# Kernel tuning notes

Measured on AMD Instinct MI355X. Metric: run time of the kernel, lower is better.

## Reference

```python
import jax, jax.numpy as jnp
import numpy as np

N, E, G = 50000, 800000, 500          # nodes, edges, graphs
NFEAT, NHID, EFEAT = 128, 128, 16
L, NCLASS = 4, 10
BN_EPS = 1e-5


def setup_inputs() -> dict:
    key = jax.random.key(0)
    ks = jax.random.split(key, 10)
    w = lambda k, shape: (jax.random.normal(k, shape, jnp.float32) * 0.05)
    return {
        "h": jax.random.normal(ks[0], (N, NFEAT), jnp.float32),
        "edge_attr": jax.random.normal(ks[1], (E, EFEAT), jnp.float32),
        "edge_index": jax.random.randint(ks[2], (2, E), 0, N),
        "edge_feat_mat": jnp.zeros((1,), jnp.int32),   # placeholder (unused by simplified conv)
        "pair_info": jnp.zeros((1,), jnp.int32),       # placeholder (unused by simplified conv)
        "batch": jnp.sort(jax.random.randint(ks[3], (N,), 0, G)),
        "emb_W": w(ks[4], (NFEAT, NHID)), "emb_b": jnp.zeros((NHID,), jnp.float32),
        "conv_W": w(ks[5], (L, NHID, NHID)), "conv_b": jnp.zeros((L, NHID), jnp.float32),
        "conv_We": w(ks[6], (L, EFEAT, NHID)), "conv_be": jnp.zeros((L, NHID), jnp.float32),
        "bn_gamma": jnp.ones((L, NHID), jnp.float32), "bn_beta": jnp.zeros((L, NHID), jnp.float32),
        "jk_W": w(ks[7], (L + 1, NHID, NCLASS)), "jk_b": jnp.zeros((L + 1, NCLASS), jnp.float32),
    }


def _conv(h, edge_attr, src, dst, W, b, We, be):
    # GIN-style message passing: gather src features, add projected edge feats,
    # scatter-add into dst, then a dense transform of (self + aggregate).
    msg = h[src] + edge_attr @ We + be                      # [E, NHID]
    agg = jax.ops.segment_sum(msg, dst, num_segments=h.shape[0])  # [N, NHID]
    return (h + agg) @ W + b


def _batch_norm(x, gamma, beta):
    mu = jnp.mean(x, axis=0)
    var = jnp.mean(jnp.square(x - mu), axis=0)  # biased, as in torch BN training
    return (x - mu) * jax.lax.rsqrt(var + BN_EPS) * gamma + beta


def reference(h, edge_attr, edge_index, edge_feat_mat, pair_info, batch,
              emb_W, emb_b, conv_W, conv_b, conv_We, conv_be,
              bn_gamma, bn_beta, jk_W, jk_b):
    src, dst = edge_index[0], edge_index[1]
    h = h @ emb_W + emb_b                                   # embedding_h
    h_list = [h]
    for layer in range(L):
        z = _conv(h, edge_attr, src, dst,
                  conv_W[layer], conv_b[layer], conv_We[layer], conv_be[layer])
        z = _batch_norm(z, bn_gamma[layer], bn_beta[layer])
        z = jax.nn.relu(z)
        h = z + h_list[layer]                               # residual (dropout p=0)
        h_list.append(h)
    # JK: sum of per-layer linear heads applied to global_add_pool
    out = jnp.zeros((G, NCLASS), jnp.float32)
    for layer in range(L + 1):
        pooled = jax.ops.segment_sum(h_list[layer], batch, num_segments=G)  # [G, NHID]
        out = out + pooled @ jk_W[layer] + jk_b[layer]
    return out
```

## Files before the change

kernel.cpp:

```cpp
#include <hip/hip_runtime.h>

#define NH 128
#define LAYERS 4
#define BW 128
#define CHUNK 4096

typedef __attribute__((ext_vector_type(8))) short short8;
typedef __attribute__((ext_vector_type(4))) float f32x4;

__device__ __forceinline__ unsigned short f2bf(float f) {
    unsigned u = __float_as_uint(f);
    u += 0x7fffu + ((u >> 16) & 1u);
    return (unsigned short)(u >> 16);
}
__device__ __forceinline__ float bflo(unsigned u) { return __uint_as_float(u << 16); }
__device__ __forceinline__ float bfhi(unsigned u) { return __uint_as_float(u & 0xffff0000u); }
__device__ __forceinline__ unsigned packbf(float x, float y) {
    return (unsigned)f2bf(x) | ((unsigned)f2bf(y) << 16);
}

__global__ __launch_bounds__(256) void bhist_kernel(const int* __restrict__ dst, int E,
                                                    int* __restrict__ gH, int NBKT, int NCH,
                                                    const int* __restrict__ batch,
                                                    int* __restrict__ gstart, int N, int G) {
    __shared__ int hist[512];
    int b = blockIdx.x, t = threadIdx.x;
    for (int i = t; i < NBKT; i += 256) hist[i] = 0;
    __syncthreads();
    int base = b * CHUNK, end = min(base + CHUNK, E);
    for (int e = base + t; e < end; e += 256)
        atomicAdd(&hist[dst[e] >> 7], 1);
    __syncthreads();
    for (int i = t; i < NBKT; i += 256) gH[i * NCH + b] = hist[i];

    for (int i = b * 256 + t; i < N; i += gridDim.x * 256) {
        int bb = batch[i];
        int prev = (i == 0) ? -1 : batch[i - 1];
        for (int g = prev + 1; g <= bb; ++g) gstart[g] = i;
        if (i == N - 1)
            for (int g = bb + 1; g <= G; ++g) gstart[g] = N;
    }
}

__global__ __launch_bounds__(256) void block_sum_kernel(const int* __restrict__ deg,
                                                        int* __restrict__ bsum, int n) {
    __shared__ int red[256];
    int t = threadIdx.x;
    int base = blockIdx.x * 1024;
    int s = 0;
#pragma unroll
    for (int i = 0; i < 4; ++i) {
        int idx = base + i * 256 + t;
        if (idx < n) s += deg[idx];
    }
    red[t] = s;
    __syncthreads();
    for (int off = 128; off > 0; off >>= 1) {
        if (t < off) red[t] += red[t + off];
        __syncthreads();
    }
    if (t == 0) bsum[blockIdx.x] = red[0];
}

__global__ __launch_bounds__(1024) void scan_partials_kernel(int* __restrict__ bsum, int nb,
                                                             int* __restrict__ total_out, int n) {
    __shared__ int part[1024];
    int t = threadIdx.x;
    int v = (t < nb) ? bsum[t] : 0;
    part[t] = v;
    __syncthreads();
    for (int off = 1; off < 1024; off <<= 1) {
        int u = (t >= off) ? part[t - off] : 0;
        __syncthreads();
        part[t] += u;
        __syncthreads();
    }
    if (t < nb) bsum[t] = part[t] - v;
    if (t == 1023) total_out[n] = part[1023];
}

__global__ __launch_bounds__(256) void local_scan_kernel(const int* __restrict__ deg,
                                                         const int* __restrict__ bsum,
                                                         int* __restrict__ outA, int n) {
    __shared__ int part[256];
    int t = threadIdx.x;
    int base = blockIdx.x * 1024 + t * 4;
    int v0 = 0, v1 = 0, v2 = 0, v3 = 0;
    if (base + 3 < n) {
        int4 v = *(const int4*)(deg + base);
        v0 = v.x; v1 = v.y; v2 = v.z; v3 = v.w;
    } else {
        if (base + 0 < n) v0 = deg[base + 0];
        if (base + 1 < n) v1 = deg[base + 1];
        if (base + 2 < n) v2 = deg[base + 2];
        if (base + 3 < n) v3 = deg[base + 3];
    }
    int tsum = v0 + v1 + v2 + v3;
    part[t] = tsum;
    __syncthreads();
    for (int off = 1; off < 256; off <<= 1) {
        int u = (t >= off) ? part[t - off] : 0;
        __syncthreads();
        part[t] += u;
        __syncthreads();
    }
    int run = bsum[blockIdx.x] + part[t] - tsum;
    int r0 = run, r1 = run + v0, r2 = r1 + v1, r3 = r2 + v2;
    if (base + 3 < n) {
        *(int4*)(outA + base) = make_int4(r0, r1, r2, r3);
    } else {
        if (base + 0 < n) outA[base + 0] = r0;
        if (base + 1 < n) outA[base + 1] = r1;
        if (base + 2 < n) outA[base + 2] = r2;
        if (base + 3 < n) outA[base + 3] = r3;
    }
}

__global__ __launch_bounds__(256) void bplace_kernel(const int* __restrict__ src,
                                                     const int* __restrict__ dst, int E,
                                                     const int* __restrict__ gOff,
                                                     int NBKT, int NCH,
                                                     int2* __restrict__ bkt) {
    __shared__ int cur[512];
    int b = blockIdx.x, t = threadIdx.x;
    for (int i = t; i < NBKT; i += 256) cur[i] = gOff[i * NCH + b];
    __syncthreads();
    int base = b * CHUNK, end = min(base + CHUNK, E);
    for (int e = base + t; e < end; e += 256) {
        int d = dst[e];
        int p = atomicAdd(&cur[d >> 7], 1);
        bkt[p] = make_int2(src[e], ((d & (BW - 1)) << 25) | e);
    }
}

__global__ __launch_bounds__(256) void bfinal_kernel(const int2* __restrict__ bkt,
                                                     const int* __restrict__ gOff, int NCH,
                                                     int* __restrict__ row_start,
                                                     int2* __restrict__ pk,
                                                     int N, int E) {
    __shared__ int cnt[BW], par[BW];
    int b = blockIdx.x, t = threadIdx.x;
    int s = gOff[b * NCH];
    int e = (b + 1 < (int)gridDim.x) ? gOff[(b + 1) * NCH] : E;
    if (t < BW) cnt[t] = 0;
    __syncthreads();
    for (int p = s + t; p < e; p += 256)
        atomicAdd(&cnt[(unsigned)bkt[p].y >> 25], 1);
    __syncthreads();
    if (t < BW) par[t] = cnt[t];
    __syncthreads();
    for (int off = 1; off < BW; off <<= 1) {
        int u = (t < BW && t >= off) ? par[t - off] : 0;
        __syncthreads();
        if (t < BW) par[t] += u;
        __syncthreads();
    }
    int node = b * BW + t;
    if (t < BW) {
        int excl = par[t] - cnt[t];
        if (node <= N) row_start[node] = s + excl;
        cnt[t] = s + excl;
    }
    if (b == 0 && t == 0) row_start[N] = E;
    __syncthreads();
    for (int p = s + t; p < e; p += 256) {
        int2 v = bkt[p];
        int dloc = (unsigned)v.y >> 25;
        int pos = atomicAdd(&cnt[dloc], 1);
        pk[pos] = make_int2(v.x, v.y & 0x1FFFFFF);
    }
}

__global__ __launch_bounds__(256) void easum_kernel(const float* __restrict__ edge_attr,
                                                    const int2* __restrict__ pk,
                                                    const int* __restrict__ row_start,
                                                    float* __restrict__ easum, int N) {
    int t = threadIdx.x;
    int node = blockIdx.x * 16 + (t >> 4);
    int k = t & 15;
    if (node >= N) return;
    int rs = row_start[node], re = row_start[node + 1];
    float acc = 0.f;
    for (int p = rs; p < re; ++p)
        acc += edge_attr[(size_t)pk[p].y * 16 + k];
    easum[node * 16 + k] = acc;
}

__global__ __launch_bounds__(256) void aggregate_kernel(
    const unsigned* __restrict__ hbfu, const int2* __restrict__ pk,
    const int* __restrict__ row_start, const float* __restrict__ easum,
    const float* __restrict__ We, const float* __restrict__ be,
    unsigned* __restrict__ xbfu, int N) {
    __shared__ float2 WeL[16 * 64];
    int t = threadIdx.x;
    const float2* Wg2 = (const float2*)We;
    for (int i = t; i < 16 * 64; i += 256) WeL[i] = Wg2[i];
    __syncthreads();

    int wave = t >> 6, lane = t & 63;
    int n = blockIdx.x * 4 + wave;
    if (n >= N) return;
    unsigned uself = hbfu[(size_t)n * 64 + lane];
    float2 acc = make_float2(bflo(uself), bfhi(uself));
    float2 acc2 = make_float2(0.f, 0.f);
    float2 acc3 = make_float2(0.f, 0.f);
    float2 acc4 = make_float2(0.f, 0.f);
    int rs = row_start[n], re = row_start[n + 1];
    float myea = (lane < 16) ? easum[n * 16 + lane] : 0.f;

    for (int base = rs; base < re; base += 64) {
        int cnt = min(64, re - base);
        int myS = (base + lane < re) ? pk[base + lane].x : 0;
        int j = 0;
        for (; j + 15 < cnt; j += 16) {
            int s0 = __shfl(myS, j);      int s1 = __shfl(myS, j + 1);
            int s2 = __shfl(myS, j + 2);  int s3 = __shfl(myS, j + 3);
            int s4 = __shfl(myS, j + 4);  int s5 = __shfl(myS, j + 5);
            int s6 = __shfl(myS, j + 6);  int s7 = __shfl(myS, j + 7);
            int s8 = __shfl(myS, j + 8);  int s9 = __shfl(myS, j + 9);
            int sa = __shfl(myS, j + 10); int sb = __shfl(myS, j + 11);
            int sc = __shfl(myS, j + 12); int sd = __shfl(myS, j + 13);
            int se = __shfl(myS, j + 14); int sf = __shfl(myS, j + 15);
            unsigned u0 = hbfu[(size_t)s0 * 64 + lane];
            unsigned u1 = hbfu[(size_t)s1 * 64 + lane];
            unsigned u2 = hbfu[(size_t)s2 * 64 + lane];
            unsigned u3 = hbfu[(size_t)s3 * 64 + lane];
            unsigned u4 = hbfu[(size_t)s4 * 64 + lane];
            unsigned u5 = hbfu[(size_t)s5 * 64 + lane];
            unsigned u6 = hbfu[(size_t)s6 * 64 + lane];
            unsigned u7 = hbfu[(size_t)s7 * 64 + lane];
            unsigned u8 = hbfu[(size_t)s8 * 64 + lane];
            unsigned u9 = hbfu[(size_t)s9 * 64 + lane];
            unsigned ua = hbfu[(size_t)sa * 64 + lane];
            unsigned ub = hbfu[(size_t)sb * 64 + lane];
            unsigned uc = hbfu[(size_t)sc * 64 + lane];
            unsigned ud = hbfu[(size_t)sd * 64 + lane];
            unsigned ue = hbfu[(size_t)se * 64 + lane];
            unsigned uf = hbfu[(size_t)sf * 64 + lane];
            acc.x  += bflo(u0) + bflo(u1) + bflo(u2) + bflo(u3);
            acc.y  += bfhi(u0) + bfhi(u1) + bfhi(u2) + bfhi(u3);
            acc2.x += bflo(u4) + bflo(u5) + bflo(u6) + bflo(u7);
            acc2.y += bfhi(u4) + bfhi(u5) + bfhi(u6) + bfhi(u7);
            acc3.x += bflo(u8) + bflo(u9) + bflo(ua) + bflo(ub);
            acc3.y += bfhi(u8) + bfhi(u9) + bfhi(ua) + bfhi(ub);
            acc4.x += bflo(uc) + bflo(ud) + bflo(ue) + bflo(uf);
            acc4.y += bfhi(uc) + bfhi(ud) + bfhi(ue) + bfhi(uf);
        }
        for (; j + 3 < cnt; j += 4) {
            int s0 = __shfl(myS, j);
            int s1 = __shfl(myS, j + 1);
            int s2 = __shfl(myS, j + 2);
            int s3 = __shfl(myS, j + 3);
            unsigned u0 = hbfu[(size_t)s0 * 64 + lane];
            unsigned u1 = hbfu[(size_t)s1 * 64 + lane];
            unsigned u2 = hbfu[(size_t)s2 * 64 + lane];
            unsigned u3 = hbfu[(size_t)s3 * 64 + lane];
            acc.x += bflo(u0) + bflo(u1) + bflo(u2) + bflo(u3);
            acc.y += bfhi(u0) + bfhi(u1) + bfhi(u2) + bfhi(u3);
        }
        for (; j < cnt; ++j) {
            int s = __shfl(myS, j);
            unsigned u = hbfu[(size_t)s * 64 + lane];
            acc.x += bflo(u);
            acc.y += bfhi(u);
        }
    }
    acc.x += (acc2.x + acc3.x) + acc4.x;
    acc.y += (acc2.y + acc3.y) + acc4.y;

    float degf = (float)(re - rs);
    float2 be2 = ((const float2*)be)[lane];
#pragma unroll
    for (int k = 0; k < 16; ++k) {
        float e = __shfl(myea, k);
        float2 w = WeL[k * 64 + lane];
        acc.x = fmaf(e, w.x, acc.x);
        acc.y = fmaf(e, w.y, acc.y);
    }
    acc.x += degf * be2.x;
    acc.y += degf * be2.y;
    xbfu[(size_t)n * 64 + lane] = packbf(acc.x, acc.y);
}

__global__ __launch_bounds__(256) void gemm_mfma_kernel(
    const unsigned short* __restrict__ Abf, const float* __restrict__ Af32,
    const float* __restrict__ W, const float* __restrict__ bias,
    float* __restrict__ Zf, unsigned short* __restrict__ Zbf,
    int N, float* __restrict__ bnsum, float* __restrict__ bnsumsq) {
    __shared__ unsigned short Wl[128 * 128];
    __shared__ float bnL[2 * NH];
    int t = threadIdx.x;
    for (int i = t; i < 128 * 64; i += 256) {
        float2 w2 = ((const float2*)W)[i];
        int k = i >> 6, n = (i & 63) * 2;
        int kc = k >> 5, quad = (k >> 3) & 3, j = k & 7;
        int base = (((n >> 4) * 4 + kc) * 4 + quad) * 128 + j;
        Wl[base + ((n & 15) << 3)] = f2bf(w2.x);
        Wl[base + (((n + 1) & 15) << 3)] = f2bf(w2.y);
    }
    if (t < 2 * NH) bnL[t] = 0.f;
    __syncthreads();

    int wave = t >> 6, lane = t & 63;
    int quad = lane >> 4, ln = lane & 15;
    int row0 = blockIdx.x * 128 + wave * 32;

    f32x4 acc[2][8];
#pragma unroll
    for (int nt = 0; nt < 8; ++nt) {
        float bv = bias[nt * 16 + ln];
        acc[0][nt] = (f32x4){bv, bv, bv, bv};
        acc[1][nt] = (f32x4){bv, bv, bv, bv};
    }

    for (int kc = 0; kc < 4; ++kc) {
        short8 afr[2];
        if (Af32) {
#pragma unroll
            for (int mt = 0; mt < 2; ++mt) {
                int ar = row0 + mt * 16 + ln; if (ar >= N) ar = N - 1;
                const float4* ap = (const float4*)(Af32 + (size_t)ar * NH + kc * 32 + quad * 8);
                float4 a0 = ap[0], a1 = ap[1];
                short8 v;
                v[0] = (short)f2bf(a0.x); v[1] = (short)f2bf(a0.y);
                v[2] = (short)f2bf(a0.z); v[3] = (short)f2bf(a0.w);
                v[4] = (short)f2bf(a1.x); v[5] = (short)f2bf(a1.y);
                v[6] = (short)f2bf(a1.z); v[7] = (short)f2bf(a1.w);
                afr[mt] = v;
            }
        } else {
#pragma unroll
            for (int mt = 0; mt < 2; ++mt) {
                int ar = row0 + mt * 16 + ln; if (ar >= N) ar = N - 1;
                afr[mt] = *(const short8*)(Abf + (size_t)ar * NH + kc * 32 + quad * 8);
            }
        }
#pragma unroll
        for (int nt = 0; nt < 8; ++nt) {
            short8 bfr = *(const short8*)(Wl + ((nt * 4 + kc) * 4 + quad) * 128 + ln * 8);
            acc[0][nt] = __builtin_amdgcn_mfma_f32_16x16x32_bf16(afr[0], bfr, acc[0][nt], 0, 0, 0);
            acc[1][nt] = __builtin_amdgcn_mfma_f32_16x16x32_bf16(afr[1], bfr, acc[1][nt], 0, 0, 0);
        }
    }

#pragma unroll
    for (int mt = 0; mt < 2; ++mt)
#pragma unroll
        for (int r = 0; r < 4; ++r) {
            int row = row0 + mt * 16 + quad * 4 + r;
            if (row < N) {
#pragma unroll
                for (int nt = 0; nt < 8; ++nt) {
                    int col = nt * 16 + ln;
                    float v = acc[mt][nt][r];
                    if (Zf) Zf[(size_t)row * NH + col] = v;
                    if (Zbf) Zbf[(size_t)row * NH + col] = f2bf(v);
                }
            }
        }

    if (bnsum) {
#pragma unroll
        for (int nt = 0; nt < 8; ++nt) {
            float s = 0.f, q = 0.f;
#pragma unroll
            for (int mt = 0; mt < 2; ++mt)
#pragma unroll
                for (int r = 0; r < 4; ++r) {
                    int row = row0 + mt * 16 + quad * 4 + r;
                    if (row < N) { float v = acc[mt][nt][r]; s += v; q += v * v; }
                }
            s += __shfl_xor(s, 16); s += __shfl_xor(s, 32);
            q += __shfl_xor(q, 16); q += __shfl_xor(q, 32);
            if (quad == 0) {
                atomicAdd(&bnL[nt * 16 + ln], s);
                atomicAdd(&bnL[NH + nt * 16 + ln], q);
            }
        }
        __syncthreads();
        if (t < NH) {
            atomicAdd(&bnsum[t], bnL[t]);
            atomicAdd(&bnsumsq[t], bnL[NH + t]);
        }
    }
}

__global__ __launch_bounds__(256) void update_pool_kernel(
    const unsigned* __restrict__ zbfu, float* __restrict__ h, unsigned* __restrict__ hbfu,
    const float* __restrict__ bnsum, const float* __restrict__ bnsumsq,
    const float* __restrict__ gamma, const float* __restrict__ beta,
    float invN, const int* __restrict__ gstart, float* __restrict__ pooled) {
    int g = blockIdx.x, t = threadIdx.x;
    __shared__ float scL[NH], shL[NH];
    __shared__ float2 red[256];
    if (t < NH) {
        float mu = bnsum[t] * invN;
        float var = fmaf(bnsumsq[t], invN, -mu * mu);
        float sc = gamma[t] * rsqrtf(var + 1e-5f);
        scL[t] = sc;
        shL[t] = beta[t] - mu * sc;
    }
    __syncthreads();
    int s = gstart[g], e = gstart[g + 1];
    int c2 = t & 63, half = t >> 6;
    float2 sc = make_float2(scL[2 * c2], scL[2 * c2 + 1]);
    float2 sh = make_float2(shL[2 * c2], shL[2 * c2 + 1]);
    float2 pacc = make_float2(0.f, 0.f);
    for (int n = s + half; n < e; n += 4) {
        size_t i = (size_t)n * 64 + c2;
        unsigned zu = zbfu[i];
        float2 hv = ((float2*)h)[i];
        float rx = fmaxf(fmaf(bflo(zu), sc.x, sh.x), 0.f) + hv.x;
        float ry = fmaxf(fmaf(bfhi(zu), sc.y, sh.y), 0.f) + hv.y;
        ((float2*)h)[i] = make_float2(rx, ry);
        hbfu[i] = packbf(rx, ry);
        pacc.x += rx; pacc.y += ry;
    }
    red[t] = pacc;
    __syncthreads();
    if (t < 64) {
        float2 a = red[t], b = red[t + 64], c = red[t + 128], d = red[t + 192];
        ((float2*)pooled)[(size_t)g * 64 + c2] =
            make_float2((a.x + b.x) + (c.x + d.x), (a.y + b.y) + (c.y + d.y));
    }
}

__global__ __launch_bounds__(256) void pool_kernel(
    const float* __restrict__ h, const int* __restrict__ gstart,
    float* __restrict__ pooled, int G) {
    int g = blockIdx.x;
    int t = threadIdx.x;
    int s = gstart[g], e = gstart[g + 1];
    int c = t & 127, half = t >> 7;
    float acc = 0.f;
    for (int n = s + half; n < e; n += 2)
        acc += h[(size_t)n * NH + c];
    __shared__ float red[256];
    red[t] = acc;
    __syncthreads();
    if (t < NH) pooled[(size_t)g * NH + t] = red[t] + red[t + NH];
}

__global__ void jk_kernel(const float* __restrict__ pooled, const float* __restrict__ jkW,
                          const float* __restrict__ jkb, float* __restrict__ out, int G) {
    int idx = blockIdx.x * blockDim.x + threadIdx.x;
    if (idx >= G * 10) return;
    int g = idx / 10, c = idx % 10;
    float acc = 0.f;
    for (int l = 0; l < LAYERS + 1; ++l) {
        acc += jkb[l * 10 + c];
        const float* pg = pooled + ((size_t)l * G + g) * NH;
        const float* wl = jkW + (size_t)l * NH * 10 + c;
        float s = 0.f;
#pragma unroll 16
        for (int k = 0; k < NH; ++k) s = fmaf(pg[k], wl[k * 10], s);
        acc += s;
    }
    out[idx] = acc;
}

extern "C" void kernel_launch(void* const* d_in, const int* in_sizes, int n_in,
                              void* d_out, int out_size, void* d_ws, size_t ws_size,
                              hipStream_t stream) {
    const float* h_in      = (const float*)d_in[0];
    const float* edge_attr = (const float*)d_in[1];
    const int*   edge_idx  = (const int*)d_in[2];
    const int*   batch     = (const int*)d_in[5];
    const float* emb_W     = (const float*)d_in[6];
    const float* emb_b     = (const float*)d_in[7];
    const float* conv_W    = (const float*)d_in[8];
    const float* conv_b    = (const float*)d_in[9];
    const float* conv_We   = (const float*)d_in[10];
    const float* conv_be   = (const float*)d_in[11];
    const float* bn_gamma  = (const float*)d_in[12];
    const float* bn_beta   = (const float*)d_in[13];
    const float* jk_W      = (const float*)d_in[14];
    const float* jk_b      = (const float*)d_in[15];
    float* out = (float*)d_out;

    const int N = in_sizes[0] / NH;
    const int E = in_sizes[1] / 16;
    const int G = out_size / 10;
    const int NBKT = (N + BW - 1) / BW;
    const int NCH  = (E + CHUNK - 1) / CHUNK;
    const int NTOT = NBKT * NCH;
    const int NBW  = (NTOT + 1023) / 1024;

    const int* src = edge_idx;
    const int* dst = edge_idx + E;

    size_t off = 0;
    auto alloc = [&](size_t bytes) -> void* {
        void* p = (char*)d_ws + off;
        off += (bytes + 255) & ~(size_t)255;
        return p;
    };
    float* hbuf = (float*)alloc((size_t)N * NH * 4);
    unsigned short* hbf = (unsigned short*)alloc((size_t)N * NH * 2);
    unsigned short* xbf = (unsigned short*)alloc((size_t)N * NH * 2);
    unsigned short* zbf = (unsigned short*)alloc((size_t)N * NH * 2);
    float* pooled  = (float*)alloc((size_t)(LAYERS + 1) * G * NH * 4);
    float* easum   = (float*)alloc((size_t)N * 16 * 4);
    size_t zero_off = off;
    float* bnsum   = (float*)alloc((size_t)LAYERS * NH * 4);
    float* bnsumsq = (float*)alloc((size_t)LAYERS * NH * 4);
    size_t zero_bytes = off - zero_off;
    int* gH        = (int*)alloc((size_t)(NTOT + 1) * 4);
    int* bsumW     = (int*)alloc((size_t)NBW * 4);
    int* gstart    = (int*)alloc((size_t)(G + 1) * 4);
    int* row_start = (int*)alloc((size_t)(N + 1) * 4);
    int2* bkt      = (int2*)alloc((size_t)E * 8);
    int2* pk       = (int2*)alloc((size_t)E * 8);
    (void)ws_size; (void)n_in;

    hipMemsetAsync((char*)d_ws + zero_off, 0, zero_bytes, stream);

    bhist_kernel<<<NCH, 256, 0, stream>>>(dst, E, gH, NBKT, NCH, batch, gstart, N, G);
    block_sum_kernel<<<NBW, 256, 0, stream>>>(gH, bsumW, NTOT);
    scan_partials_kernel<<<1, 1024, 0, stream>>>(bsumW, NBW, gH, NTOT);
    local_scan_kernel<<<NBW, 256, 0, stream>>>(gH, bsumW, gH, NTOT);
    bplace_kernel<<<NCH, 256, 0, stream>>>(src, dst, E, gH, NBKT, NCH, bkt);
    bfinal_kernel<<<NBKT, 256, 0, stream>>>(bkt, gH, NCH, row_start, pk, N, E);
    easum_kernel<<<(N + 15) / 16, 256, 0, stream>>>(edge_attr, pk, row_start, easum, N);

    dim3 gemm_grid((N + 127) / 128);
    dim3 agg_grid((N + 3) / 4);

    gemm_mfma_kernel<<<gemm_grid, 256, 0, stream>>>(
        nullptr, h_in, emb_W, emb_b, hbuf, hbf, N, nullptr, nullptr);
    pool_kernel<<<G, 256, 0, stream>>>(hbuf, gstart, pooled, G);

    for (int l = 0; l < LAYERS; ++l) {
        aggregate_kernel<<<agg_grid, 256, 0, stream>>>(
            (const unsigned*)hbf, pk, row_start, easum,
            conv_We + (size_t)l * 16 * NH, conv_be + (size_t)l * NH,
            (unsigned*)xbf, N);
        gemm_mfma_kernel<<<gemm_grid, 256, 0, stream>>>(
            xbf, nullptr, conv_W + (size_t)l * NH * NH, conv_b + (size_t)l * NH,
            nullptr, zbf, N, bnsum + (size_t)l * NH, bnsumsq + (size_t)l * NH);
        update_pool_kernel<<<G, 256, 0, stream>>>(
            (const unsigned*)zbf, hbuf, (unsigned*)hbf,
            bnsum + (size_t)l * NH, bnsumsq + (size_t)l * NH,
            bn_gamma + (size_t)l * NH, bn_beta + (size_t)l * NH,
            1.0f / (float)N, gstart, pooled + (size_t)(l + 1) * G * NH);
    }

    jk_kernel<<<(G * 10 + 255) / 256, 256, 0, stream>>>(pooled, jk_W, jk_b, out, G);
}
```

Before: 634.9 us.

## Drop fp32 hidden-state buffer and pre-swizzle weights once into bf16

The fp32 residual state buffer is removed, so the residual stream is kept only in bf16. The update kernel now reads and writes bf16 h, and pooling reads bf16, which roughly halves the bytes moved per layer for h. Separately, a small kernel converts and swizzles all five weight matrices to bf16 once, so each GEMM block does a plain vector copy into shared memory instead of converting per block. The cost is accuracy: the residual stream is now rounded to bf16 at every layer and errors accumulate.

```diff
diff --git a/kernel.cpp b/kernel.cpp
--- a/kernel.cpp
+++ b/kernel.cpp
@@ -17,6 +17,20 @@
 __device__ __forceinline__ float bfhi(unsigned u) { return __uint_as_float(u & 0xffff0000u); }
 __device__ __forceinline__ unsigned packbf(float x, float y) {
     return (unsigned)f2bf(x) | ((unsigned)f2bf(y) << 16);
+}
+
+__global__ void wswz_kernel(const float* __restrict__ emb_W, const float* __restrict__ conv_W,
+                            unsigned short* __restrict__ Wsw) {
+    int idx = blockIdx.x * 256 + threadIdx.x;
+    if (idx >= 5 * 8192) return;
+    int m = idx >> 13, i = idx & 8191;
+    const float* W = (m == 0) ? emb_W : conv_W + (size_t)(m - 1) * 16384;
+    float2 w2 = ((const float2*)W)[i];
+    int k = i >> 6, n = (i & 63) * 2;
+    int kc = k >> 5, quad = (k >> 3) & 3, j = k & 7;
+    int base = m * 16384 + (((n >> 4) * 4 + kc) * 4 + quad) * 128 + j;
+    Wsw[base + ((n & 15) << 3)] = f2bf(w2.x);
+    Wsw[base + (((n + 1) & 15) << 3)] = f2bf(w2.y);
 }
 
 __global__ __launch_bounds__(256) void bhist_kernel(const int* __restrict__ dst, int E,
@@ -284,19 +298,16 @@
 
 __global__ __launch_bounds__(256) void gemm_mfma_kernel(
     const unsigned short* __restrict__ Abf, const float* __restrict__ Af32,
-    const float* __restrict__ W, const float* __restrict__ bias,
-    float* __restrict__ Zf, unsigned short* __restrict__ Zbf,
+    const unsigned short* __restrict__ Wsw, const float* __restrict__ bias,
+    unsigned short* __restrict__ Zbf,
     int N, float* __restrict__ bnsum, float* __restrict__ bnsumsq) {
     __shared__ unsigned short Wl[128 * 128];
     __shared__ float bnL[2 * NH];
     int t = threadIdx.x;
-    for (int i = t; i < 128 * 64; i += 256) {
-        float2 w2 = ((const float2*)W)[i];
-        int k = i >> 6, n = (i & 63) * 2;
-        int kc = k >> 5, quad = (k >> 3) & 3, j = k & 7;
-        int base = (((n >> 4) * 4 + kc) * 4 + quad) * 128 + j;
-        Wl[base + ((n & 15) << 3)] = f2bf(w2.x);
-        Wl[base + (((n + 1) & 15) << 3)] = f2bf(w2.y);
+    {
+        const float4* Wg = (const float4*)Wsw;
+        float4* Wl4 = (float4*)Wl;
+        for (int i = t; i < 2048; i += 256) Wl4[i] = Wg[i];
     }
     if (t < 2 * NH) bnL[t] = 0.f;
     __syncthreads();
@@ -350,12 +361,8 @@
             int row = row0 + mt * 16 + quad * 4 + r;
             if (row < N) {
 #pragma unroll
-                for (int nt = 0; nt < 8; ++nt) {
-                    int col = nt * 16 + ln;
-                    float v = acc[mt][nt][r];
-                    if (Zf) Zf[(size_t)row * NH + col] = v;
-                    if (Zbf) Zbf[(size_t)row * NH + col] = f2bf(v);
-                }
+                for (int nt = 0; nt < 8; ++nt)
+                    Zbf[(size_t)row * NH + nt * 16 + ln] = f2bf(acc[mt][nt][r]);
             }
         }
 
@@ -386,7 +393,7 @@
 }
 
 __global__ __launch_bounds__(256) void update_pool_kernel(
-    const unsigned* __restrict__ zbfu, float* __restrict__ h, unsigned* __restrict__ hbfu,
+    const unsigned* __restrict__ zbfu, unsigned* __restrict__ hbfu,
     const float* __restrict__ bnsum, const float* __restrict__ bnsumsq,
     const float* __restrict__ gamma, const float* __restrict__ beta,
     float invN, const int* __restrict__ gstart, float* __restrict__ pooled) {
@@ -409,10 +416,9 @@
     for (int n = s + half; n < e; n += 4) {
         size_t i = (size_t)n * 64 + c2;
         unsigned zu = zbfu[i];
-        float2 hv = ((float2*)h)[i];
-        float rx = fmaxf(fmaf(bflo(zu), sc.x, sh.x), 0.f) + hv.x;
-        float ry = fmaxf(fmaf(bfhi(zu), sc.y, sh.y), 0.f) + hv.y;
-        ((float2*)h)[i] = make_float2(rx, ry);
+        unsigned hu = hbfu[i];
+        float rx = fmaxf(fmaf(bflo(zu), sc.x, sh.x), 0.f) + bflo(hu);
+        float ry = fmaxf(fmaf(bfhi(zu), sc.y, sh.y), 0.f) + bfhi(hu);
         hbfu[i] = packbf(rx, ry);
         pacc.x += rx; pacc.y += ry;
     }
@@ -426,19 +432,25 @@
 }
 
 __global__ __launch_bounds__(256) void pool_kernel(
-    const float* __restrict__ h, const int* __restrict__ gstart,
+    const unsigned* __restrict__ hbfu, const int* __restrict__ gstart,
     float* __restrict__ pooled, int G) {
-    int g = blockIdx.x;
-    int t = threadIdx.x;
+    int g = blockIdx.x, t = threadIdx.x;
+    __shared__ float2 red[256];
     int s = gstart[g], e = gstart[g + 1];
-    int c = t & 127, half = t >> 7;
-    float acc = 0.f;
-    for (int n = s + half; n < e; n += 2)
-        acc += h[(size_t)n * NH + c];
-    __shared__ float red[256];
-    red[t] = acc;
-    __syncthreads();
-    if (t < NH) pooled[(size_t)g * NH + t] = red[t] + red[t + NH];
+    int c2 = t & 63, half = t >> 6;
+    float2 pacc = make_float2(0.f, 0.f);
+    for (int n = s + half; n < e; n += 4) {
+        unsigned u = hbfu[(size_t)n * 64 + c2];
+        pacc.x += bflo(u);
+        pacc.y += bfhi(u);
+    }
+    red[t] = pacc;
+    __syncthreads();
+    if (t < 64) {
+        float2 a = red[t], b = red[t + 64], c = red[t + 128], d = red[t + 192];
+        ((float2*)pooled)[(size_t)g * 64 + c2] =
+            make_float2((a.x + b.x) + (c.x + d.x), (a.y + b.y) + (c.y + d.y));
+    }
 }
 
 __global__ void jk_kernel(const float* __restrict__ pooled, const float* __restrict__ jkW,
@@ -495,10 +507,10 @@
         off += (bytes + 255) & ~(size_t)255;
         return p;
     };
-    float* hbuf = (float*)alloc((size_t)N * NH * 4);
     unsigned short* hbf = (unsigned short*)alloc((size_t)N * NH * 2);
     unsigned short* xbf = (unsigned short*)alloc((size_t)N * NH * 2);
     unsigned short* zbf = (unsigned short*)alloc((size_t)N * NH * 2);
+    unsigned short* Wsw = (unsigned short*)alloc((size_t)5 * NH * NH * 2);
     float* pooled  = (float*)alloc((size_t)(LAYERS + 1) * G * NH * 4);
     float* easum   = (float*)alloc((size_t)N * 16 * 4);
     size_t zero_off = off;
@@ -515,6 +527,8 @@
 
     hipMemsetAsync((char*)d_ws + zero_off, 0, zero_bytes, stream);
 
+    wswz_kernel<<<(5 * 8192 + 255) / 256, 256, 0, stream>>>(emb_W, conv_W, Wsw);
+
     bhist_kernel<<<NCH, 256, 0, stream>>>(dst, E, gH, NBKT, NCH, batch, gstart, N, G);
     block_sum_kernel<<<NBW, 256, 0, stream>>>(gH, bsumW, NTOT);
     scan_partials_kernel<<<1, 1024, 0, stream>>>(bsumW, NBW, gH, NTOT);
@@ -527,8 +541,8 @@
     dim3 agg_grid((N + 3) / 4);
 
     gemm_mfma_kernel<<<gemm_grid, 256, 0, stream>>>(
-        nullptr, h_in, emb_W, emb_b, hbuf, hbf, N, nullptr, nullptr);
-    pool_kernel<<<G, 256, 0, stream>>>(hbuf, gstart, pooled, G);
+        nullptr, h_in, Wsw, emb_b, hbf, N, nullptr, nullptr);
+    pool_kernel<<<G, 256, 0, stream>>>((const unsigned*)hbf, gstart, pooled, G);
 
     for (int l = 0; l < LAYERS; ++l) {
         aggregate_kernel<<<agg_grid, 256, 0, stream>>>(
@@ -536,10 +550,10 @@
             conv_We + (size_t)l * 16 * NH, conv_be + (size_t)l * NH,
             (unsigned*)xbf, N);
         gemm_mfma_kernel<<<gemm_grid, 256, 0, stream>>>(
-            xbf, nullptr, conv_W + (size_t)l * NH * NH, conv_b + (size_t)l * NH,
-            nullptr, zbf, N, bnsum + (size_t)l * NH, bnsumsq + (size_t)l * NH);
+            xbf, nullptr, Wsw + (size_t)(l + 1) * NH * NH, conv_b + (size_t)l * NH,
+            zbf, N, bnsum + (size_t)l * NH, bnsumsq + (size_t)l * NH);
         update_pool_kernel<<<G, 256, 0, stream>>>(
-            (const unsigned*)zbf, hbuf, (unsigned*)hbf,
+            (const unsigned*)zbf, (unsigned*)hbf,
             bnsum + (size_t)l * NH, bnsumsq + (size_t)l * NH,
             bn_gamma + (size_t)l * NH, bn_beta + (size_t)l * NH,
             1.0f / (float)N, gstart, pooled + (size_t)(l + 1) * G * NH);
```

Measured after the change: 549.1 us. -13.5%, faster.
